# Optimization experiments

Hardware: AMD Instinct MI355X
Metric: run time of the kernel (lower is better)

Reference implementation:

```python
import jax, jax.numpy as jnp
import numpy as np

B, K = 2048, 256
ED = RD = HD = 256
AD = ED + RD          # action_dim = 512
IN = ED + HD + RD     # 768
NUM_E, NUM_R = 100000, 500
HUGE = jnp.float32(1e31)  # ops.HUGE_INT


def setup_inputs() -> dict:
    key = jax.random.key(0)
    ks = jax.random.split(key, 12)
    s = 0.05  # keep logits in a sane range
    E = jax.random.normal(ks[0], (B, ED), jnp.float32)
    H = jax.random.normal(ks[1], (B, HD), jnp.float32)
    Q = jax.random.normal(ks[2], (B, RD), jnp.float32)
    W1 = jax.random.normal(ks[3], (AD, IN), jnp.float32) * s
    b1 = jnp.zeros((AD,), jnp.float32)
    W2 = jax.random.normal(ks[4], (AD, AD), jnp.float32) * s
    b2 = jnp.zeros((AD,), jnp.float32)
    emb_r = jax.random.normal(ks[5], (NUM_R, RD), jnp.float32) * s
    emb_e = jax.random.normal(ks[6], (NUM_E, ED), jnp.float32) * s
    # binary action mask (variable-size action spaces, padded); col 0 always valid
    action_mask = (jax.random.uniform(ks[7], (B, K)) > 0.3).astype(jnp.float32)
    action_mask = action_mask.at[:, 0].set(1.0)
    r_space = jax.random.randint(ks[8], (B, K), 0, NUM_R)
    e_space = jax.random.randint(ks[9], (B, K), 0, NUM_E)
    return {"E": E, "H": H, "Q": Q, "W1": W1, "b1": b1, "W2": W2, "b2": b2,
            "emb_r": emb_r, "emb_e": emb_e, "action_mask": action_mask,
            "r_space": r_space, "e_space": e_space}


def reference(E, H, Q, W1, b1, W2, b2, emb_r, emb_e, action_mask, r_space, e_space):
    # state MLP: X = W2Dropout(W2(relu(W1(cat([E, H, Q])))))  (dropout = identity at eval)
    X = jnp.concatenate([E, H, Q], axis=-1)           # [B, IN]
    X = jax.nn.relu(X @ W1.T + b1)                    # [B, AD]
    X2 = X @ W2.T + b2                                # [B, AD]
    # gather action embeddings: A = cat([emb_r[r], emb_e[e]])  [B, K, AD]
    A = jnp.concatenate([emb_r[r_space], emb_e[e_space]], axis=-1)
    # masked softmax over action space
    scores = jnp.einsum('bkd,bd->bk', A, X2) - (1.0 - action_mask) * HUGE
    action_dist = jax.nn.softmax(scores, axis=-1)     # [B, K]
    entropy = -jnp.sum(action_dist * jnp.log(action_dist + 1e-20), axis=-1)  # [B]
    return action_dist, entropy
```

## Files before the change

### kernel.cpp

```cpp
#include <hip/hip_runtime.h>
#include <hip/hip_bf16.h>
#include <math.h>

#define B_   2048
#define K_   256
#define AD_  512
#define IN_  768
#define NR_  500
#define NRP_ 512

typedef __attribute__((ext_vector_type(8))) short short8;
typedef __attribute__((ext_vector_type(4))) float float4v;

__device__ __forceinline__ unsigned short f2bf(float f) {
    unsigned int u = __float_as_uint(f);
    unsigned int r = u + 0x7FFF + ((u >> 16) & 1);
    return (unsigned short)(r >> 16);
}

#define X_N4  (B_ * IN_ / 4)
#define W1_N4 (AD_ * IN_ / 4)
#define W2_N4 (AD_ * AD_ / 4)
#define ER_N4 (NR_ * 256 / 4)
#define PREP_TOTAL (X_N4 + W1_N4 + W2_N4 + ER_N4)
__global__ __launch_bounds__(256) void prep_kernel(
    const float* __restrict__ E, const float* __restrict__ H,
    const float* __restrict__ Q, const float* __restrict__ W1,
    const float* __restrict__ W2, const float* __restrict__ emb_r,
    ushort* __restrict__ Xb, ushort* __restrict__ W1b,
    ushort* __restrict__ W2b, ushort* __restrict__ emb_rb)
{
    int t = blockIdx.x * 256 + threadIdx.x;
    const float* src; ushort* dst; int off;
    if (t < X_N4) {
        const int base = t * 4;
        const int row = base / IN_, col = base % IN_;
        src = (col < 256) ? &E[row * 256 + col]
            : (col < 512) ? &H[row * 256 + col - 256]
                          : &Q[row * 256 + col - 512];
        const float4 v = *(const float4*)src;
        ushort4 o;
        o.x = f2bf(v.x); o.y = f2bf(v.y); o.z = f2bf(v.z); o.w = f2bf(v.w);
        *(ushort4*)&Xb[base] = o;
        return;
    }
    t -= X_N4;
    if (t < W1_N4)                 { src = W1;    dst = W1b;    off = t; }
    else if (t < W1_N4 + W2_N4)    { src = W2;    dst = W2b;    off = t - W1_N4; }
    else if (t < W1_N4 + W2_N4 + ER_N4) { src = emb_r; dst = emb_rb; off = t - W1_N4 - W2_N4; }
    else return;
    const float4 v = *(const float4*)&src[off * 4];
    ushort4 o;
    o.x = f2bf(v.x); o.y = f2bf(v.y); o.z = f2bf(v.z); o.w = f2bf(v.w);
    *(ushort4*)&dst[off * 4] = o;
}

template<int K, bool RELU, bool OUT_BF16, bool BIAS, bool EMIT_RHALF>
__global__ __launch_bounds__(256) void gemm_bf16_kernel(
    const ushort* __restrict__ A, const ushort* __restrict__ Bw,
    const float* __restrict__ bias, ushort* __restrict__ outb,
    float* __restrict__ outf, ushort* __restrict__ rhalf)
{
    constexpr int PITCH = 40;
    __shared__ ushort Asl[64 * PITCH];
    __shared__ ushort Bsl[64 * PITCH];
    const int tid = threadIdx.x;
    const int lane = tid & 63, w = tid >> 6;
    const int n0 = blockIdx.x * 64, m0 = blockIdx.y * 64;
    const int lrow = tid >> 2, lcg = (tid & 3) * 8;
    const int q = lane >> 4, l16 = lane & 15;

    const ushort* aptr = &A[(size_t)(m0 + lrow) * K + lcg];
    const ushort* bptr = &Bw[(size_t)(n0 + lrow) * K + lcg];
    short8 ra = *(const short8*)aptr;
    short8 rb = *(const short8*)bptr;

    float4v acc[4] = {};
    for (int k0 = 0; k0 < K; k0 += 32) {
        *(short8*)&Asl[lrow * PITCH + lcg] = ra;
        *(short8*)&Bsl[lrow * PITCH + lcg] = rb;
        __syncthreads();
        if (k0 + 32 < K) {
            ra = *(const short8*)(aptr + k0 + 32);
            rb = *(const short8*)(bptr + k0 + 32);
        }
        const short8 af = *(const short8*)&Asl[(w * 16 + l16) * PITCH + q * 8];
        #pragma unroll
        for (int jn = 0; jn < 4; ++jn) {
            const short8 bf = *(const short8*)&Bsl[(jn * 16 + l16) * PITCH + q * 8];
            acc[jn] = __builtin_amdgcn_mfma_f32_16x16x32_bf16(af, bf, acc[jn], 0, 0, 0);
        }
        __syncthreads();
    }
    #pragma unroll
    for (int jn = 0; jn < 4; ++jn) {
        const int n = n0 + jn * 16 + l16;
        const float bn = BIAS ? bias[n] : 0.0f;
        #pragma unroll
        for (int r = 0; r < 4; ++r) {
            const int m = m0 + w * 16 + q * 4 + r;
            float c = acc[jn][r] + bn;
            if (RELU) c = fmaxf(c, 0.0f);
            if (OUT_BF16) outb[(size_t)m * AD_ + n] = f2bf(c);
            else          outf[(size_t)m * AD_ + n] = c;
            if (EMIT_RHALF && n < 256) rhalf[(size_t)m * 256 + n] = f2bf(c);
        }
    }
}

__global__ __launch_bounds__(256) void scores_kernel(
    const float* __restrict__ X2, const float* __restrict__ R,
    const float* __restrict__ emb_e, const float* __restrict__ mask,
    const int* __restrict__ r_space, const int* __restrict__ e_space,
    float* __restrict__ dist, float* __restrict__ entropy)
{
    const int b = blockIdx.x;
    const int tid = threadIdx.x;
    const int lane = tid & 63, wid = tid >> 6;

    __shared__ int   s_e[K_];
    __shared__ float s_dot[K_];
    __shared__ float s_red[12];

    s_e[tid] = e_space[b * K_ + tid];
    const int   r_mine = r_space[b * K_ + tid];
    const float mk     = mask[b * K_ + tid];
    const float bias   = R[(size_t)b * NRP_ + r_mine] - (1.0f - mk) * 1e31f;
    const float4 xe = *(const float4*)&X2[(size_t)b * AD_ + 256 + lane * 4];
    __syncthreads();

    const int kbase = wid * 64;
    #pragma unroll
    for (int kk = 0; kk < 64; kk += 8) {
        float p[8];
        #pragma unroll
        for (int u = 0; u < 8; ++u) {
            const int e = s_e[kbase + kk + u];
            const float4 ae = *(const float4*)&emb_e[(size_t)e * 256 + lane * 4];
            p[u] = ae.x * xe.x + ae.y * xe.y + ae.z * xe.z + ae.w * xe.w;
        }
        #pragma unroll
        for (int off = 32; off >= 1; off >>= 1) {
            #pragma unroll
            for (int u = 0; u < 8; ++u) p[u] += __shfl_down(p[u], off);
        }
        if (lane == 0) {
            #pragma unroll
            for (int u = 0; u < 8; ++u) s_dot[kbase + kk + u] = p[u];
        }
    }
    __syncthreads();

    const float v = s_dot[tid] + bias;

    float m = v;
    #pragma unroll
    for (int off = 32; off >= 1; off >>= 1) m = fmaxf(m, __shfl_down(m, off));
    if (lane == 0) s_red[wid] = m;
    __syncthreads();
    if (tid == 0)
        s_red[8] = fmaxf(fmaxf(s_red[0], s_red[1]), fmaxf(s_red[2], s_red[3]));
    __syncthreads();
    const float bmax = s_red[8];

    const float ev = __expf(v - bmax);
    float s = ev;
    float t = ev * (v - bmax);
    #pragma unroll
    for (int off = 32; off >= 1; off >>= 1) {
        s += __shfl_down(s, off);
        t += __shfl_down(t, off);
    }
    if (lane == 0) { s_red[wid] = s; s_red[4 + wid] = t; }
    __syncthreads();
    if (tid == 0) {
        s_red[9]  = s_red[0] + s_red[1] + s_red[2] + s_red[3];
        s_red[10] = s_red[4] + s_red[5] + s_red[6] + s_red[7];
    }
    __syncthreads();
    const float ssum = s_red[9];

    dist[(size_t)b * K_ + tid] = ev / ssum;
    if (tid == 0)
        entropy[b] = logf(ssum) - s_red[10] / ssum;
}

extern "C" void kernel_launch(void* const* d_in, const int* in_sizes, int n_in,
                              void* d_out, int out_size, void* d_ws, size_t ws_size,
                              hipStream_t stream) {
    const float* E     = (const float*)d_in[0];
    const float* H     = (const float*)d_in[1];
    const float* Q     = (const float*)d_in[2];
    const float* W1    = (const float*)d_in[3];
    const float* b1    = (const float*)d_in[4];
    const float* W2    = (const float*)d_in[5];
    const float* b2    = (const float*)d_in[6];
    const float* emb_r = (const float*)d_in[7];
    const float* emb_e = (const float*)d_in[8];
    const float* mask  = (const float*)d_in[9];
    const int* r_space = (const int*)d_in[10];
    const int* e_space = (const int*)d_in[11];

    float* out_dist = (float*)d_out;
    float* out_ent  = out_dist + (size_t)B_ * K_;

    char* ws = (char*)d_ws;
    ushort* Xb     = (ushort*)ws;  ws += (size_t)B_ * IN_ * 2;
    ushort* W1b    = (ushort*)ws;  ws += (size_t)AD_ * IN_ * 2;
    ushort* W2b    = (ushort*)ws;  ws += (size_t)AD_ * AD_ * 2;
    ushort* emb_rb = (ushort*)ws;  ws += (size_t)NRP_ * 256 * 2;
    ushort* H1b    = (ushort*)ws;  ws += (size_t)B_ * AD_ * 2;
    float*  X2     = (float*)ws;   ws += (size_t)B_ * AD_ * 4;
    ushort* X2rb   = (ushort*)ws;  ws += (size_t)B_ * 256 * 2;
    float*  Rt     = (float*)ws;   ws += (size_t)B_ * NRP_ * 4;

    prep_kernel<<<(PREP_TOTAL + 255) / 256, 256, 0, stream>>>(
        E, H, Q, W1, W2, emb_r, Xb, W1b, W2b, emb_rb);

    dim3 g(AD_ / 64, B_ / 64);
    gemm_bf16_kernel<IN_, true,  true,  true,  false><<<g, 256, 0, stream>>>(
        Xb, W1b, b1, H1b, nullptr, nullptr);
    gemm_bf16_kernel<AD_, false, false, true,  true ><<<g, 256, 0, stream>>>(
        H1b, W2b, b2, nullptr, X2, X2rb);
    gemm_bf16_kernel<256, false, false, false, false><<<dim3(NRP_ / 64, B_ / 64), 256, 0, stream>>>(
        X2rb, emb_rb, nullptr, nullptr, Rt, nullptr);

    scores_kernel<<<B_, 256, 0, stream>>>(X2, Rt, emb_e, mask,
                                          r_space, e_space, out_dist, out_ent);
}
```

Measured before the change: 253.1 us.

## Convert entity embeddings to bf16 for gathers and double-buffer GEMM tiles

The prep kernel now converts the whole 100k x 256 entity embedding table to bf16 on every call. The scores kernel then gathers half-width rows, with each half-wave handling one action row, so the random-gather traffic is halved. Separately, the bf16 GEMM moves to a 64-wide K step with double-buffered shared memory and one barrier per step. The trade-off is a full-table conversion pass of about 150 MB of traffic per call, plus reduced precision on the entity dot products.

```diff
diff --git a/kernel.cpp b/kernel.cpp
--- a/kernel.cpp
+++ b/kernel.cpp
@@ -8,6 +8,7 @@
 #define IN_  768
 #define NR_  500
 #define NRP_ 512
+#define NE_  100000
 
 typedef __attribute__((ext_vector_type(8))) short short8;
 typedef __attribute__((ext_vector_type(4))) float float4v;
@@ -17,42 +18,52 @@
     unsigned int r = u + 0x7FFF + ((u >> 16) & 1);
     return (unsigned short)(r >> 16);
 }
-
+__device__ __forceinline__ float bf2f(short s) {
+    return __uint_as_float(((unsigned int)(unsigned short)s) << 16);
+}
+
+#define EE_N4 (NE_ * 256 / 4)
 #define X_N4  (B_ * IN_ / 4)
 #define W1_N4 (AD_ * IN_ / 4)
 #define W2_N4 (AD_ * AD_ / 4)
 #define ER_N4 (NR_ * 256 / 4)
-#define PREP_TOTAL (X_N4 + W1_N4 + W2_N4 + ER_N4)
+#define PREP_TOTAL (EE_N4 + X_N4 + W1_N4 + W2_N4 + ER_N4)
 __global__ __launch_bounds__(256) void prep_kernel(
     const float* __restrict__ E, const float* __restrict__ H,
     const float* __restrict__ Q, const float* __restrict__ W1,
     const float* __restrict__ W2, const float* __restrict__ emb_r,
+    const float* __restrict__ emb_e,
     ushort* __restrict__ Xb, ushort* __restrict__ W1b,
-    ushort* __restrict__ W2b, ushort* __restrict__ emb_rb)
+    ushort* __restrict__ W2b, ushort* __restrict__ emb_rb,
+    ushort* __restrict__ emb_eb)
 {
     int t = blockIdx.x * 256 + threadIdx.x;
     const float* src; ushort* dst; int off;
-    if (t < X_N4) {
-        const int base = t * 4;
-        const int row = base / IN_, col = base % IN_;
-        src = (col < 256) ? &E[row * 256 + col]
-            : (col < 512) ? &H[row * 256 + col - 256]
-                          : &Q[row * 256 + col - 512];
-        const float4 v = *(const float4*)src;
-        ushort4 o;
-        o.x = f2bf(v.x); o.y = f2bf(v.y); o.z = f2bf(v.z); o.w = f2bf(v.w);
-        *(ushort4*)&Xb[base] = o;
-        return;
-    }
-    t -= X_N4;
-    if (t < W1_N4)                 { src = W1;    dst = W1b;    off = t; }
-    else if (t < W1_N4 + W2_N4)    { src = W2;    dst = W2b;    off = t - W1_N4; }
-    else if (t < W1_N4 + W2_N4 + ER_N4) { src = emb_r; dst = emb_rb; off = t - W1_N4 - W2_N4; }
-    else return;
-    const float4 v = *(const float4*)&src[off * 4];
+    if (t < EE_N4) { src = emb_e; dst = emb_eb; off = t; }
+    else {
+        t -= EE_N4;
+        if (t < X_N4) {
+            const int base = t * 4;
+            const int row = base / IN_, col = base % IN_;
+            src = (col < 256) ? &E[row * 256 + col]
+                : (col < 512) ? &H[row * 256 + col - 256]
+                              : &Q[row * 256 + col - 512];
+            const float4 v = *(const float4*)src;
+            ushort4 o;
+            o.x = f2bf(v.x); o.y = f2bf(v.y); o.z = f2bf(v.z); o.w = f2bf(v.w);
+            *(ushort4*)&Xb[base] = o;
+            return;
+        }
+        t -= X_N4;
+        if (t < W1_N4)                 { src = W1;    dst = W1b;    off = t; }
+        else if (t < W1_N4 + W2_N4)    { src = W2;    dst = W2b;    off = t - W1_N4; }
+        else if (t < W1_N4 + W2_N4 + ER_N4) { src = emb_r; dst = emb_rb; off = t - W1_N4 - W2_N4; }
+        else return;
+    }
+    const float4 v = *(const float4*)&src[(size_t)off * 4];
     ushort4 o;
     o.x = f2bf(v.x); o.y = f2bf(v.y); o.z = f2bf(v.z); o.w = f2bf(v.w);
-    *(ushort4*)&dst[off * 4] = o;
+    *(ushort4*)&dst[(size_t)off * 4] = o;
 }
 
 template<int K, bool RELU, bool OUT_BF16, bool BIAS, bool EMIT_RHALF>
@@ -61,36 +72,54 @@
     const float* __restrict__ bias, ushort* __restrict__ outb,
     float* __restrict__ outf, ushort* __restrict__ rhalf)
 {
-    constexpr int PITCH = 40;
-    __shared__ ushort Asl[64 * PITCH];
-    __shared__ ushort Bsl[64 * PITCH];
+    constexpr int PITCH = 72;
+    __shared__ ushort Asl[2][64 * PITCH];
+    __shared__ ushort Bsl[2][64 * PITCH];
     const int tid = threadIdx.x;
     const int lane = tid & 63, w = tid >> 6;
     const int n0 = blockIdx.x * 64, m0 = blockIdx.y * 64;
-    const int lrow = tid >> 2, lcg = (tid & 3) * 8;
+    const int lrow = tid >> 2, lcg = (tid & 3) * 16;
     const int q = lane >> 4, l16 = lane & 15;
 
     const ushort* aptr = &A[(size_t)(m0 + lrow) * K + lcg];
     const ushort* bptr = &Bw[(size_t)(n0 + lrow) * K + lcg];
-    short8 ra = *(const short8*)aptr;
-    short8 rb = *(const short8*)bptr;
+
+    short8 ra0 = *(const short8*)aptr;
+    short8 ra1 = *(const short8*)(aptr + 8);
+    short8 rb0 = *(const short8*)bptr;
+    short8 rb1 = *(const short8*)(bptr + 8);
+    *(short8*)&Asl[0][lrow * PITCH + lcg]     = ra0;
+    *(short8*)&Asl[0][lrow * PITCH + lcg + 8] = ra1;
+    *(short8*)&Bsl[0][lrow * PITCH + lcg]     = rb0;
+    *(short8*)&Bsl[0][lrow * PITCH + lcg + 8] = rb1;
 
     float4v acc[4] = {};
-    for (int k0 = 0; k0 < K; k0 += 32) {
-        *(short8*)&Asl[lrow * PITCH + lcg] = ra;
-        *(short8*)&Bsl[lrow * PITCH + lcg] = rb;
-        __syncthreads();
-        if (k0 + 32 < K) {
-            ra = *(const short8*)(aptr + k0 + 32);
-            rb = *(const short8*)(bptr + k0 + 32);
-        }
-        const short8 af = *(const short8*)&Asl[(w * 16 + l16) * PITCH + q * 8];
-        #pragma unroll
-        for (int jn = 0; jn < 4; ++jn) {
-            const short8 bf = *(const short8*)&Bsl[(jn * 16 + l16) * PITCH + q * 8];
-            acc[jn] = __builtin_amdgcn_mfma_f32_16x16x32_bf16(af, bf, acc[jn], 0, 0, 0);
-        }
-        __syncthreads();
+    int buf = 0;
+    __syncthreads();
+    for (int k0 = 0; k0 < K; k0 += 64) {
+        if (k0 + 64 < K) {
+            ra0 = *(const short8*)(aptr + k0 + 64);
+            ra1 = *(const short8*)(aptr + k0 + 64 + 8);
+            rb0 = *(const short8*)(bptr + k0 + 64);
+            rb1 = *(const short8*)(bptr + k0 + 64 + 8);
+        }
+        #pragma unroll
+        for (int kh = 0; kh < 64; kh += 32) {
+            const short8 af = *(const short8*)&Asl[buf][(w * 16 + l16) * PITCH + kh + q * 8];
+            #pragma unroll
+            for (int jn = 0; jn < 4; ++jn) {
+                const short8 bfr = *(const short8*)&Bsl[buf][(jn * 16 + l16) * PITCH + kh + q * 8];
+                acc[jn] = __builtin_amdgcn_mfma_f32_16x16x32_bf16(af, bfr, acc[jn], 0, 0, 0);
+            }
+        }
+        if (k0 + 64 < K) {
+            *(short8*)&Asl[buf ^ 1][lrow * PITCH + lcg]     = ra0;
+            *(short8*)&Asl[buf ^ 1][lrow * PITCH + lcg + 8] = ra1;
+            *(short8*)&Bsl[buf ^ 1][lrow * PITCH + lcg]     = rb0;
+            *(short8*)&Bsl[buf ^ 1][lrow * PITCH + lcg + 8] = rb1;
+            __syncthreads();
+            buf ^= 1;
+        }
     }
     #pragma unroll
     for (int jn = 0; jn < 4; ++jn) {
@@ -110,13 +139,14 @@
 
 __global__ __launch_bounds__(256) void scores_kernel(
     const float* __restrict__ X2, const float* __restrict__ R,
-    const float* __restrict__ emb_e, const float* __restrict__ mask,
+    const ushort* __restrict__ emb_eb, const float* __restrict__ mask,
     const int* __restrict__ r_space, const int* __restrict__ e_space,
     float* __restrict__ dist, float* __restrict__ entropy)
 {
     const int b = blockIdx.x;
     const int tid = threadIdx.x;
     const int lane = tid & 63, wid = tid >> 6;
+    const int half = lane >> 5, l32 = lane & 31;
 
     __shared__ int   s_e[K_];
     __shared__ float s_dot[K_];
@@ -126,27 +156,32 @@
     const int   r_mine = r_space[b * K_ + tid];
     const float mk     = mask[b * K_ + tid];
     const float bias   = R[(size_t)b * NRP_ + r_mine] - (1.0f - mk) * 1e31f;
-    const float4 xe = *(const float4*)&X2[(size_t)b * AD_ + 256 + lane * 4];
+    const float4 x0 = *(const float4*)&X2[(size_t)b * AD_ + 256 + l32 * 8];
+    const float4 x1 = *(const float4*)&X2[(size_t)b * AD_ + 256 + l32 * 8 + 4];
     __syncthreads();
 
     const int kbase = wid * 64;
     #pragma unroll
-    for (int kk = 0; kk < 64; kk += 8) {
+    for (int kk = 0; kk < 64; kk += 16) {
         float p[8];
         #pragma unroll
         for (int u = 0; u < 8; ++u) {
-            const int e = s_e[kbase + kk + u];
-            const float4 ae = *(const float4*)&emb_e[(size_t)e * 256 + lane * 4];
-            p[u] = ae.x * xe.x + ae.y * xe.y + ae.z * xe.z + ae.w * xe.w;
-        }
-        #pragma unroll
-        for (int off = 32; off >= 1; off >>= 1) {
+            const int row = kbase + kk + u * 2 + half;
+            const int e = s_e[row];
+            const short8 ae = *(const short8*)&emb_eb[(size_t)e * 256 + l32 * 8];
+            p[u] = bf2f(ae[0]) * x0.x + bf2f(ae[1]) * x0.y
+                 + bf2f(ae[2]) * x0.z + bf2f(ae[3]) * x0.w
+                 + bf2f(ae[4]) * x1.x + bf2f(ae[5]) * x1.y
+                 + bf2f(ae[6]) * x1.z + bf2f(ae[7]) * x1.w;
+        }
+        #pragma unroll
+        for (int off = 16; off >= 1; off >>= 1) {
             #pragma unroll
-            for (int u = 0; u < 8; ++u) p[u] += __shfl_down(p[u], off);
-        }
-        if (lane == 0) {
+            for (int u = 0; u < 8; ++u) p[u] += __shfl_down(p[u], off, 32);
+        }
+        if (l32 == 0) {
             #pragma unroll
-            for (int u = 0; u < 8; ++u) s_dot[kbase + kk + u] = p[u];
+            for (int u = 0; u < 8; ++u) s_dot[kbase + kk + u * 2 + half] = p[u];
         }
     }
     __syncthreads();
@@ -209,13 +244,14 @@
     ushort* W1b    = (ushort*)ws;  ws += (size_t)AD_ * IN_ * 2;
     ushort* W2b    = (ushort*)ws;  ws += (size_t)AD_ * AD_ * 2;
     ushort* emb_rb = (ushort*)ws;  ws += (size_t)NRP_ * 256 * 2;
+    ushort* emb_eb = (ushort*)ws;  ws += (size_t)NE_ * 256 * 2;
     ushort* H1b    = (ushort*)ws;  ws += (size_t)B_ * AD_ * 2;
     float*  X2     = (float*)ws;   ws += (size_t)B_ * AD_ * 4;
     ushort* X2rb   = (ushort*)ws;  ws += (size_t)B_ * 256 * 2;
     float*  Rt     = (float*)ws;   ws += (size_t)B_ * NRP_ * 4;
 
     prep_kernel<<<(PREP_TOTAL + 255) / 256, 256, 0, stream>>>(
-        E, H, Q, W1, W2, emb_r, Xb, W1b, W2b, emb_rb);
+        E, H, Q, W1, W2, emb_r, emb_e, Xb, W1b, W2b, emb_rb, emb_eb);
 
     dim3 g(AD_ / 64, B_ / 64);
     gemm_bf16_kernel<IN_, true,  true,  true,  false><<<g, 256, 0, stream>>>(
@@ -225,6 +261,6 @@
     gemm_bf16_kernel<256, false, false, false, false><<<dim3(NRP_ / 64, B_ / 64), 256, 0, stream>>>(
         X2rb, emb_rb, nullptr, nullptr, Rt, nullptr);
 
-    scores_kernel<<<B_, 256, 0, stream>>>(X2, Rt, emb_e, mask,
+    scores_kernel<<<B_, 256, 0, stream>>>(X2, Rt, emb_eb, mask,
                                           r_space, e_space, out_dist, out_ent);
 }
```

New measurement: 242.3 us. 4.3% less time.
